# Performance work log

Hardware: AMD Instinct MI355X
Metric: run time of the kernel (lower is better)

## Reference

```python
import jax, jax.numpy as jnp
import numpy as np

N_NODES = 10000
N_EDGES = 640000
IN_CH = 128
HID = 256
OUT_CH = 10
NUM_GRAPHS = 64
EPS = 0.0  # non-trainable buffer, initial_eps=0


def setup_inputs() -> dict:
    key = jax.random.key(0)
    ks = jax.random.split(key, 12)
    x = jax.random.normal(ks[0], (N_NODES, IN_CH), dtype=jnp.float32)
    edge_index = jax.random.randint(ks[1], (2, N_EDGES), 0, N_NODES, dtype=jnp.int64)
    batch = jnp.sort(jax.random.randint(ks[2], (N_NODES,), 0, NUM_GRAPHS, dtype=jnp.int64))
    edge_weights = jax.random.uniform(ks[3], (N_EDGES,), dtype=jnp.float32)
    def lin(k, fan_in, fan_out):
        bound = 1.0 / np.sqrt(fan_in)
        kw, kb = jax.random.split(k)
        W = jax.random.uniform(kw, (fan_out, fan_in), minval=-bound, maxval=bound, dtype=jnp.float32)
        b = jax.random.uniform(kb, (fan_out,), minval=-bound, maxval=bound, dtype=jnp.float32)
        return W, b
    W1, b1 = lin(ks[4], IN_CH, HID)
    W2, b2 = lin(ks[5], HID, HID)
    W3, b3 = lin(ks[6], HID, HID)
    Wl, bl = lin(ks[7], HID, OUT_CH)
    return {"x": x, "edge_index": edge_index, "batch": batch, "edge_weights": edge_weights,
            "W1": W1, "b1": b1, "W2": W2, "b2": b2, "W3": W3, "b3": b3, "Wl": Wl, "bl": bl}


def _ginw_conv(x, edge_index, edge_weights, W, b):
    # message: edge_weight * x_j (source nodes), aggregated by add at target i
    src, dst = edge_index[0], edge_index[1]
    msg = edge_weights[:, None] * x[src]           # [E, F]
    agg = jax.ops.segment_sum(msg, dst, num_segments=N_NODES)  # [N, F]
    out = agg + (1.0 + EPS) * x
    return out @ W.T + b


def reference(x, edge_index, batch, edge_weights, W1, b1, W2, b2, W3, b3, Wl, bl):
    h = jax.nn.relu(_ginw_conv(x, edge_index, edge_weights, W1, b1))
    h = jax.nn.relu(_ginw_conv(h, edge_index, edge_weights, W2, b2))
    h = jax.nn.relu(_ginw_conv(h, edge_index, edge_weights, W3, b3))
    # global mean pool over graphs
    sums = jax.ops.segment_sum(h, batch, num_segments=NUM_GRAPHS)        # [G, HID]
    cnts = jax.ops.segment_sum(jnp.ones((N_NODES,), h.dtype), batch, num_segments=NUM_GRAPHS)
    pooled = sums / jnp.maximum(cnts, 1.0)[:, None]
    return pooled @ Wl.T + bl
```

## Files before the change

### kernel.cpp

```cpp
#include <hip/hip_runtime.h>
#include <hip/hip_fp16.h>

namespace {
constexpr int NN   = 10000;
constexpr int NE   = 640000;
constexpr int INC  = 128;
constexpr int HIDC = 256;
constexpr int OUTC = 10;
constexpr int NG   = 64;
constexpr int DCAP = 128;
}

typedef __attribute__((ext_vector_type(8))) _Float16 half8;
typedef __attribute__((ext_vector_type(4))) float f32x4;
typedef __attribute__((ext_vector_type(4))) ushort u16x4;

__device__ __forceinline__ ushort f2h(float f) { return __half_as_ushort(__float2half(f)); }
__device__ __forceinline__ float h2f(ushort u) { return __half2float(__ushort_as_half(u)); }

__global__ __launch_bounds__(256) void prep_kernel(int* __restrict__ cnt,
                                                   const float* __restrict__ x,
                                                   ushort* __restrict__ xh,
                                                   const float* __restrict__ W1,
                                                   ushort* __restrict__ w1h,
                                                   const float* __restrict__ W2,
                                                   ushort* __restrict__ w2h,
                                                   const float* __restrict__ W3,
                                                   ushort* __restrict__ w3h) {
    const int gt = blockIdx.x * 256 + threadIdx.x;
    const int gs = gridDim.x * 256;
    for (int i = gt; i < NN; i += gs) cnt[i] = 0;
    {
        const int n4 = NN * INC / 4;
        for (int i = gt; i < n4; i += gs) {
            f32x4 v = __builtin_nontemporal_load((const f32x4*)x + i);
            u16x4 o;
#pragma unroll
            for (int j = 0; j < 4; j++) o[j] = f2h(v[j]);
            __builtin_nontemporal_store(o, (u16x4*)xh + i);
        }
    }
    {
        const int n4 = HIDC * INC / 4;
        for (int i = gt; i < n4; i += gs) {
            f32x4 v = __builtin_nontemporal_load((const f32x4*)W1 + i);
            u16x4 o;
#pragma unroll
            for (int j = 0; j < 4; j++) o[j] = f2h(v[j]);
            __builtin_nontemporal_store(o, (u16x4*)w1h + i);
        }
    }
    {
        const int n4 = HIDC * HIDC / 4;
        for (int i = gt; i < n4; i += gs) {
            f32x4 v = __builtin_nontemporal_load((const f32x4*)W2 + i);
            u16x4 o;
#pragma unroll
            for (int j = 0; j < 4; j++) o[j] = f2h(v[j]);
            __builtin_nontemporal_store(o, (u16x4*)w2h + i);
            f32x4 v3 = __builtin_nontemporal_load((const f32x4*)W3 + i);
            u16x4 o3;
#pragma unroll
            for (int j = 0; j < 4; j++) o3[j] = f2h(v3[j]);
            __builtin_nontemporal_store(o3, (u16x4*)w3h + i);
        }
    }
}

__global__ __launch_bounds__(256) void scatter_kernel(const int* __restrict__ ei,
                                                      const float* __restrict__ ew,
                                                      int* __restrict__ cnt,
                                                      uint* __restrict__ erec) {
    const int e = blockIdx.x * 256 + threadIdx.x;
    if (e >= NE) return;
    const int src = __builtin_nontemporal_load(ei + e);
    const int dst = __builtin_nontemporal_load(ei + NE + e);
    const ushort hw = __half_as_ushort(__float2half(__builtin_nontemporal_load(ew + e)));
    const int idx = atomicAdd(&cnt[dst], 1);
    if (idx < DCAP)
        erec[((size_t)dst << 7) + idx] = ((uint)src << 16) | (uint)hw;
}

__global__ __launch_bounds__(256) void gather128_kernel(const int* __restrict__ cnt,
                                                        const uint* __restrict__ erec,
                                                        const ushort* __restrict__ x,
                                                        ushort* __restrict__ out) {
    constexpr int U = 16;
    const int n = blockIdx.x * 4 + (threadIdx.x >> 6);
    const int lane = threadIdx.x & 63;
    if (n >= NN) return;
    const int beg = n << 7;
    const int end = beg + min(cnt[n], DCAP);
    const size_t loff = (size_t)lane * 2;
    const ushort* xr = x + loff;

    float a0, a1, b0 = 0.f, b1 = 0.f;
    {
        ushort2 v = *(const ushort2*)(x + (size_t)n * INC + loff);
        a0 = h2f(v.x);
        a1 = h2f(v.y);
    }

    int e = beg;
    for (; e + U <= end; e += U) {
        uint rec[U];
#pragma unroll
        for (int u = 0; u < U; u++) rec[u] = erec[e + u];
        ushort2 v[U];
#pragma unroll
        for (int u = 0; u < U; u++)
            v[u] = *(const ushort2*)(xr + (size_t)(rec[u] >> 16) * INC);
#pragma unroll
        for (int u = 0; u < U; u++) {
            const float w = h2f((ushort)(rec[u] & 0xFFFFu));
            if (u & 1) { b0 += w * h2f(v[u].x); b1 += w * h2f(v[u].y); }
            else       { a0 += w * h2f(v[u].x); a1 += w * h2f(v[u].y); }
        }
    }
    for (; e < end; e++) {
        const uint rec = erec[e];
        const float w = h2f((ushort)(rec & 0xFFFFu));
        const ushort2 v = *(const ushort2*)(xr + (size_t)(rec >> 16) * INC);
        a0 += w * h2f(v.x);
        a1 += w * h2f(v.y);
    }

    ushort2 o;
    o.x = f2h(a0 + b0);
    o.y = f2h(a1 + b1);
    *(ushort2*)(out + (size_t)n * INC + loff) = o;
}

__global__ __launch_bounds__(256) void gather_half_kernel(const int* __restrict__ cnt,
                                                          const uint* __restrict__ erec,
                                                          const ushort* __restrict__ x,
                                                          ushort* __restrict__ out) {
    constexpr int U = 16;
    const int half = blockIdx.x & 1;
    const int n = (blockIdx.x >> 1) * 4 + (threadIdx.x >> 6);
    const int lane = threadIdx.x & 63;
    if (n >= NN) return;
    const int beg = n << 7;
    const int end = beg + min(cnt[n], DCAP);
    const size_t loff = (size_t)half * 128 + lane * 2;
    const ushort* xr = x + loff;

    float a0, a1, b0 = 0.f, b1 = 0.f;
    {
        ushort2 v = *(const ushort2*)(x + (size_t)n * HIDC + loff);
        a0 = h2f(v.x);
        a1 = h2f(v.y);
    }

    int e = beg;
    for (; e + U <= end; e += U) {
        uint rec[U];
#pragma unroll
        for (int u = 0; u < U; u++) rec[u] = erec[e + u];
        ushort2 v[U];
#pragma unroll
        for (int u = 0; u < U; u++)
            v[u] = *(const ushort2*)(xr + (size_t)(rec[u] >> 16) * HIDC);
#pragma unroll
        for (int u = 0; u < U; u++) {
            const float w = h2f((ushort)(rec[u] & 0xFFFFu));
            if (u & 1) { b0 += w * h2f(v[u].x); b1 += w * h2f(v[u].y); }
            else       { a0 += w * h2f(v[u].x); a1 += w * h2f(v[u].y); }
        }
    }
    for (; e < end; e++) {
        const uint rec = erec[e];
        const float w = h2f((ushort)(rec & 0xFFFFu));
        const ushort2 v = *(const ushort2*)(xr + (size_t)(rec >> 16) * HIDC);
        a0 += w * h2f(v.x);
        a1 += w * h2f(v.y);
    }

    ushort2 o;
    o.x = f2h(a0 + b0);
    o.y = f2h(a1 + b1);
    *(ushort2*)(out + (size_t)n * HIDC + loff) = o;
}

template <int K>
__global__ __launch_bounds__(256) void mfma_gemm_kernel(const ushort* __restrict__ A,
                                                        const ushort* __restrict__ Wb,
                                                        const float* __restrict__ bias,
                                                        ushort* __restrict__ C, int M) {
    constexpr int LDW = K + 8;
    __shared__ ushort Ws[64 * LDW];
    const int tid = threadIdx.x;
    const int bm = blockIdx.x * 128;
    const int bn = blockIdx.y * 64;

    constexpr int CPR = K / 8;
    for (int idx = tid; idx < 64 * CPR; idx += 256) {
        int r = idx / CPR, c = idx % CPR;
        uint4 v = *(const uint4*)(Wb + (size_t)(bn + r) * K + c * 8);
        *(uint4*)(&Ws[r * LDW + c * 8]) = v;
    }
    __syncthreads();

    const int wave = tid >> 6;
    const int lane = tid & 63;
    const int lrow = lane & 15;
    const int lq   = lane >> 4;
    const int m0 = bm + wave * 32;

    f32x4 acc[2][4] = {};
    const int r0 = min(m0 + lrow, M - 1);
    const int r1 = min(m0 + 16 + lrow, M - 1);

    for (int k0 = 0; k0 < K; k0 += 32) {
        const int kk = k0 + lq * 8;
        half8 a0 = __builtin_nontemporal_load((const half8*)(A + (size_t)r0 * K + kk));
        half8 a1 = __builtin_nontemporal_load((const half8*)(A + (size_t)r1 * K + kk));
        half8 b[4];
#pragma unroll
        for (int j = 0; j < 4; j++)
            b[j] = *(const half8*)(&Ws[(j * 16 + lrow) * LDW + kk]);
#pragma unroll
        for (int j = 0; j < 4; j++) {
            acc[0][j] = __builtin_amdgcn_mfma_f32_16x16x32_f16(a0, b[j], acc[0][j], 0, 0, 0);
            acc[1][j] = __builtin_amdgcn_mfma_f32_16x16x32_f16(a1, b[j], acc[1][j], 0, 0, 0);
        }
    }

#pragma unroll
    for (int sub = 0; sub < 2; sub++) {
#pragma unroll
        for (int j = 0; j < 4; j++) {
            const int gn = bn + j * 16 + lrow;
            const float bv = bias[gn];
#pragma unroll
            for (int i = 0; i < 4; i++) {
                const int gm = m0 + sub * 16 + lq * 4 + i;
                if (gm < M) {
                    float v = acc[sub][j][i] + bv;
                    v = fmaxf(v, 0.0f);
                    C[(size_t)gm * HIDC + gn] = f2h(v);
                }
            }
        }
    }
}

__device__ __forceinline__ int lower_bound_batch(const int* __restrict__ batch, int val) {
    int lo = 0, hi = NN;
    while (lo < hi) {
        int mid = (lo + hi) >> 1;
        if (batch[mid] < val) lo = mid + 1;
        else hi = mid;
    }
    return lo;
}

__global__ __launch_bounds__(512) void pool_head_kernel(const ushort* __restrict__ h,
                                                        const int* __restrict__ batch,
                                                        const float* __restrict__ Wl,
                                                        const float* __restrict__ bl,
                                                        float* __restrict__ out) {
    __shared__ float s[8][HIDC];
    __shared__ float s2[OUTC][8];
    const int g = blockIdx.x;
    const int t = threadIdx.x;
    const int p = t >> 6;
    const int c0 = (t & 63) * 4;
    const int lo = lower_bound_batch(batch, g);
    const int hi = lower_bound_batch(batch, g + 1);

    float a0 = 0.f, a1 = 0.f, a2 = 0.f, a3 = 0.f;
    for (int n = lo + p; n < hi; n += 8) {
        u16x4 v = *(const u16x4*)(h + (size_t)n * HIDC + c0);
        a0 += h2f(v[0]); a1 += h2f(v[1]); a2 += h2f(v[2]); a3 += h2f(v[3]);
    }
    s[p][c0 + 0] = a0; s[p][c0 + 1] = a1; s[p][c0 + 2] = a2; s[p][c0 + 3] = a3;
    __syncthreads();

    if (t < HIDC) {
        const float inv = 1.0f / fmaxf((float)(hi - lo), 1.0f);
        float m = 0.f;
#pragma unroll
        for (int q = 0; q < 8; q++) m += s[q][t];
        s[0][t] = m * inv;
    }
    __syncthreads();

    if (t < OUTC * 8) {
        const int oc = t >> 3, q = t & 7;
        float acc = 0.f;
        for (int k = q * 32; k < q * 32 + 32; k++)
            acc += s[0][k] * Wl[(size_t)oc * HIDC + k];
        s2[oc][q] = acc;
    }
    __syncthreads();
    if (t < OUTC) {
        float acc = bl[t];
#pragma unroll
        for (int q = 0; q < 8; q++) acc += s2[t][q];
        out[(size_t)g * OUTC + t] = acc;
    }
}

extern "C" void kernel_launch(void* const* d_in, const int* in_sizes, int n_in,
                              void* d_out, int out_size, void* d_ws, size_t ws_size,
                              hipStream_t stream) {
    const float* x     = (const float*)d_in[0];
    const int*   ei    = (const int*)d_in[1];
    const int*   batch = (const int*)d_in[2];
    const float* ew    = (const float*)d_in[3];
    const float* W1    = (const float*)d_in[4];
    const float* b1    = (const float*)d_in[5];
    const float* W2    = (const float*)d_in[6];
    const float* b2    = (const float*)d_in[7];
    const float* W3    = (const float*)d_in[8];
    const float* b3    = (const float*)d_in[9];
    const float* Wl    = (const float*)d_in[10];
    const float* bl    = (const float*)d_in[11];

    char* p = (char*)d_ws;
    ushort* xh     = (ushort*)p; p += (size_t)NN * INC * 2;
    ushort* agg128 = (ushort*)p; p += (size_t)NN * INC * 2;
    ushort* agg256 = (ushort*)p; p += (size_t)NN * HIDC * 2;
    ushort* h      = (ushort*)p; p += (size_t)NN * HIDC * 2;
    ushort* w1h    = (ushort*)p; p += (size_t)HIDC * INC * 2;
    ushort* w2h    = (ushort*)p; p += (size_t)HIDC * HIDC * 2;
    ushort* w3h    = (ushort*)p; p += (size_t)HIDC * HIDC * 2;
    uint*   erec   = (uint*)p;   p += (size_t)NN * DCAP * 4;
    int*    cnt    = (int*)p;    p += (size_t)NN * 4;

    prep_kernel<<<256, 256, 0, stream>>>(cnt, x, xh, W1, w1h, W2, w2h, W3, w3h);
    scatter_kernel<<<(NE + 255) / 256, 256, 0, stream>>>(ei, ew, cnt, erec);

    const int gather_grid = (NN + 3) / 4;
    dim3 gemm_grid((NN + 127) / 128, HIDC / 64);

    gather128_kernel<<<gather_grid, 256, 0, stream>>>(cnt, erec, xh, agg128);
    mfma_gemm_kernel<INC><<<gemm_grid, 256, 0, stream>>>(agg128, w1h, b1, h, NN);

    gather_half_kernel<<<gather_grid * 2, 256, 0, stream>>>(cnt, erec, h, agg256);
    mfma_gemm_kernel<HIDC><<<gemm_grid, 256, 0, stream>>>(agg256, w2h, b2, h, NN);

    gather_half_kernel<<<gather_grid * 2, 256, 0, stream>>>(cnt, erec, h, agg256);
    mfma_gemm_kernel<HIDC><<<gemm_grid, 256, 0, stream>>>(agg256, w3h, b3, h, NN);

    pool_head_kernel<<<NG, 512, 0, stream>>>(h, batch, Wl, bl, (float*)d_out);
}
```

Before: 261.4 us.

## Restructure CSR build with LDS histograms, widen gathers, fuse pooling into final GEMM

Replaces the global-atomic edge scatter with 16 blocks that each build a shared-memory histogram of destination degrees. Each block then reserves a range per node with one global atomic and fills slots through LDS atomics, while the other blocks run the fp16 conversion of x and the weights in the same launch. The gather kernels now split each wave into two half-waves that handle alternating edges with 4-wide loads and combine them with a cross-lane shuffle. The last GEMM accumulates ReLU outputs straight into per-graph pooled sums through LDS and global float atomics, so the final h is never written back and the head kernel only reads the pooled sums. This adds float-atomic ordering nondeterminism and assumes each 128-row tile covers at most six graphs.

```diff
diff --git a/kernel.cpp b/kernel.cpp
--- a/kernel.cpp
+++ b/kernel.cpp
@@ -9,6 +9,9 @@
 constexpr int OUTC = 10;
 constexpr int NG   = 64;
 constexpr int DCAP = 128;
+constexpr int SB   = 16;
+constexpr int EPB  = NE / SB;
+constexpr int CB   = 240;
 }
 
 typedef __attribute__((ext_vector_type(8))) _Float16 half8;
@@ -18,18 +21,83 @@
 __device__ __forceinline__ ushort f2h(float f) { return __half_as_ushort(__float2half(f)); }
 __device__ __forceinline__ float h2f(ushort u) { return __half2float(__ushort_as_half(u)); }
 
-__global__ __launch_bounds__(256) void prep_kernel(int* __restrict__ cnt,
-                                                   const float* __restrict__ x,
-                                                   ushort* __restrict__ xh,
-                                                   const float* __restrict__ W1,
-                                                   ushort* __restrict__ w1h,
-                                                   const float* __restrict__ W2,
-                                                   ushort* __restrict__ w2h,
-                                                   const float* __restrict__ W3,
-                                                   ushort* __restrict__ w3h) {
+__global__ __launch_bounds__(256) void zero_kernel(int* __restrict__ deg,
+                                                   float* __restrict__ pooled) {
     const int gt = blockIdx.x * 256 + threadIdx.x;
     const int gs = gridDim.x * 256;
-    for (int i = gt; i < NN; i += gs) cnt[i] = 0;
+    for (int i = gt; i < NN; i += gs) deg[i] = 0;
+    for (int i = gt; i < NG * HIDC; i += gs) pooled[i] = 0.0f;
+}
+
+__global__ __launch_bounds__(1024) void build_kernel(const int* __restrict__ ei,
+                                                     const float* __restrict__ ew,
+                                                     int* __restrict__ deg,
+                                                     uint* __restrict__ erec,
+                                                     const float* __restrict__ x,
+                                                     ushort* __restrict__ xh,
+                                                     const float* __restrict__ W1,
+                                                     ushort* __restrict__ w1h,
+                                                     const float* __restrict__ W2,
+                                                     ushort* __restrict__ w2h,
+                                                     const float* __restrict__ W3,
+                                                     ushort* __restrict__ w3h) {
+    __shared__ int hist[NN];
+    const int t = threadIdx.x;
+    const int bid = blockIdx.x;
+
+    if (bid < SB) {
+        const int ebase = bid * EPB;
+        for (int i = t; i < NN; i += 1024) hist[i] = 0;
+        __syncthreads();
+
+        for (int it = 0; it < 10; ++it) {
+            const int vi = it * 4096 + t * 4;
+            if (vi < EPB) {
+                const int4 d4 = *(const int4*)(ei + NE + ebase + vi);
+                atomicAdd(&hist[d4.x], 1);
+                atomicAdd(&hist[d4.y], 1);
+                atomicAdd(&hist[d4.z], 1);
+                atomicAdd(&hist[d4.w], 1);
+            }
+        }
+        __syncthreads();
+
+        for (int b = t; b < NN; b += 1024) {
+            const int c = hist[b];
+            if (c > 0) hist[b] = atomicAdd(&deg[b], c);
+        }
+        __syncthreads();
+
+        for (int it = 0; it < 10; ++it) {
+            const int vi = it * 4096 + t * 4;
+            if (vi < EPB) {
+                const int e = ebase + vi;
+                const int4 s4 = *(const int4*)(ei + e);
+                const int4 d4 = *(const int4*)(ei + NE + e);
+                const float4 w4 = *(const float4*)(ew + e);
+                {
+                    const int idx = atomicAdd(&hist[d4.x], 1);
+                    if (idx < DCAP) erec[((size_t)d4.x << 7) + idx] = ((uint)s4.x << 16) | f2h(w4.x);
+                }
+                {
+                    const int idx = atomicAdd(&hist[d4.y], 1);
+                    if (idx < DCAP) erec[((size_t)d4.y << 7) + idx] = ((uint)s4.y << 16) | f2h(w4.y);
+                }
+                {
+                    const int idx = atomicAdd(&hist[d4.z], 1);
+                    if (idx < DCAP) erec[((size_t)d4.z << 7) + idx] = ((uint)s4.z << 16) | f2h(w4.z);
+                }
+                {
+                    const int idx = atomicAdd(&hist[d4.w], 1);
+                    if (idx < DCAP) erec[((size_t)d4.w << 7) + idx] = ((uint)s4.w << 16) | f2h(w4.w);
+                }
+            }
+        }
+        return;
+    }
+
+    const int gt = (bid - SB) * 1024 + t;
+    const int gs = CB * 1024;
     {
         const int n4 = NN * INC / 4;
         for (int i = gt; i < n4; i += gs) {
@@ -67,119 +135,137 @@
     }
 }
 
-__global__ __launch_bounds__(256) void scatter_kernel(const int* __restrict__ ei,
-                                                      const float* __restrict__ ew,
-                                                      int* __restrict__ cnt,
-                                                      uint* __restrict__ erec) {
-    const int e = blockIdx.x * 256 + threadIdx.x;
-    if (e >= NE) return;
-    const int src = __builtin_nontemporal_load(ei + e);
-    const int dst = __builtin_nontemporal_load(ei + NE + e);
-    const ushort hw = __half_as_ushort(__float2half(__builtin_nontemporal_load(ew + e)));
-    const int idx = atomicAdd(&cnt[dst], 1);
-    if (idx < DCAP)
-        erec[((size_t)dst << 7) + idx] = ((uint)src << 16) | (uint)hw;
-}
-
-__global__ __launch_bounds__(256) void gather128_kernel(const int* __restrict__ cnt,
+__global__ __launch_bounds__(256) void gather128_kernel(const int* __restrict__ deg,
                                                         const uint* __restrict__ erec,
                                                         const ushort* __restrict__ x,
                                                         ushort* __restrict__ out) {
-    constexpr int U = 16;
+    constexpr int U = 8;
     const int n = blockIdx.x * 4 + (threadIdx.x >> 6);
+    if (n >= NN) return;
     const int lane = threadIdx.x & 63;
-    if (n >= NN) return;
+    const int sub = lane >> 5;
+    const int cl  = lane & 31;
+    const int d = min(deg[n], DCAP);
     const int beg = n << 7;
-    const int end = beg + min(cnt[n], DCAP);
-    const size_t loff = (size_t)lane * 2;
+    const size_t loff = (size_t)cl * 4;
     const ushort* xr = x + loff;
 
-    float a0, a1, b0 = 0.f, b1 = 0.f;
+    float a0, a1, a2, a3;
     {
-        ushort2 v = *(const ushort2*)(x + (size_t)n * INC + loff);
-        a0 = h2f(v.x);
-        a1 = h2f(v.y);
-    }
-
-    int e = beg;
-    for (; e + U <= end; e += U) {
+        u16x4 v = *(const u16x4*)(x + (size_t)n * INC + loff);
+        a0 = sub ? 0.f : h2f(v[0]);
+        a1 = sub ? 0.f : h2f(v[1]);
+        a2 = sub ? 0.f : h2f(v[2]);
+        a3 = sub ? 0.f : h2f(v[3]);
+    }
+
+    int e = 0;
+    for (; e + 2 * U <= d; e += 2 * U) {
         uint rec[U];
 #pragma unroll
-        for (int u = 0; u < U; u++) rec[u] = erec[e + u];
-        ushort2 v[U];
+        for (int u = 0; u < U; u++) rec[u] = erec[beg + e + 2 * u + sub];
+        u16x4 v[U];
 #pragma unroll
         for (int u = 0; u < U; u++)
-            v[u] = *(const ushort2*)(xr + (size_t)(rec[u] >> 16) * INC);
+            v[u] = *(const u16x4*)(xr + (size_t)(rec[u] >> 16) * INC);
 #pragma unroll
         for (int u = 0; u < U; u++) {
             const float w = h2f((ushort)(rec[u] & 0xFFFFu));
-            if (u & 1) { b0 += w * h2f(v[u].x); b1 += w * h2f(v[u].y); }
-            else       { a0 += w * h2f(v[u].x); a1 += w * h2f(v[u].y); }
-        }
-    }
-    for (; e < end; e++) {
-        const uint rec = erec[e];
+            a0 += w * h2f(v[u][0]);
+            a1 += w * h2f(v[u][1]);
+            a2 += w * h2f(v[u][2]);
+            a3 += w * h2f(v[u][3]);
+        }
+    }
+    for (; e + 2 <= d; e += 2) {
+        const uint rec = erec[beg + e + sub];
         const float w = h2f((ushort)(rec & 0xFFFFu));
-        const ushort2 v = *(const ushort2*)(xr + (size_t)(rec >> 16) * INC);
-        a0 += w * h2f(v.x);
-        a1 += w * h2f(v.y);
-    }
-
-    ushort2 o;
-    o.x = f2h(a0 + b0);
-    o.y = f2h(a1 + b1);
-    *(ushort2*)(out + (size_t)n * INC + loff) = o;
-}
-
-__global__ __launch_bounds__(256) void gather_half_kernel(const int* __restrict__ cnt,
+        const u16x4 v = *(const u16x4*)(xr + (size_t)(rec >> 16) * INC);
+        a0 += w * h2f(v[0]); a1 += w * h2f(v[1]); a2 += w * h2f(v[2]); a3 += w * h2f(v[3]);
+    }
+    if (e < d && sub == 0) {
+        const uint rec = erec[beg + e];
+        const float w = h2f((ushort)(rec & 0xFFFFu));
+        const u16x4 v = *(const u16x4*)(xr + (size_t)(rec >> 16) * INC);
+        a0 += w * h2f(v[0]); a1 += w * h2f(v[1]); a2 += w * h2f(v[2]); a3 += w * h2f(v[3]);
+    }
+
+    a0 += __shfl_xor(a0, 32, 64);
+    a1 += __shfl_xor(a1, 32, 64);
+    a2 += __shfl_xor(a2, 32, 64);
+    a3 += __shfl_xor(a3, 32, 64);
+    if (sub == 0) {
+        u16x4 o;
+        o[0] = f2h(a0); o[1] = f2h(a1); o[2] = f2h(a2); o[3] = f2h(a3);
+        __builtin_nontemporal_store(o, (u16x4*)(out + (size_t)n * INC + loff));
+    }
+}
+
+__global__ __launch_bounds__(256) void gather_half_kernel(const int* __restrict__ deg,
                                                           const uint* __restrict__ erec,
                                                           const ushort* __restrict__ x,
                                                           ushort* __restrict__ out) {
-    constexpr int U = 16;
+    constexpr int U = 8;
     const int half = blockIdx.x & 1;
     const int n = (blockIdx.x >> 1) * 4 + (threadIdx.x >> 6);
+    if (n >= NN) return;
     const int lane = threadIdx.x & 63;
-    if (n >= NN) return;
+    const int sub = lane >> 5;
+    const int cl  = lane & 31;
+    const int d = min(deg[n], DCAP);
     const int beg = n << 7;
-    const int end = beg + min(cnt[n], DCAP);
-    const size_t loff = (size_t)half * 128 + lane * 2;
+    const size_t loff = (size_t)half * 128 + cl * 4;
     const ushort* xr = x + loff;
 
-    float a0, a1, b0 = 0.f, b1 = 0.f;
+    float a0, a1, a2, a3;
     {
-        ushort2 v = *(const ushort2*)(x + (size_t)n * HIDC + loff);
-        a0 = h2f(v.x);
-        a1 = h2f(v.y);
-    }
-
-    int e = beg;
-    for (; e + U <= end; e += U) {
+        u16x4 v = *(const u16x4*)(x + (size_t)n * HIDC + loff);
+        a0 = sub ? 0.f : h2f(v[0]);
+        a1 = sub ? 0.f : h2f(v[1]);
+        a2 = sub ? 0.f : h2f(v[2]);
+        a3 = sub ? 0.f : h2f(v[3]);
+    }
+
+    int e = 0;
+    for (; e + 2 * U <= d; e += 2 * U) {
         uint rec[U];
 #pragma unroll
-        for (int u = 0; u < U; u++) rec[u] = erec[e + u];
-        ushort2 v[U];
+        for (int u = 0; u < U; u++) rec[u] = erec[beg + e + 2 * u + sub];
+        u16x4 v[U];
 #pragma unroll
         for (int u = 0; u < U; u++)
-            v[u] = *(const ushort2*)(xr + (size_t)(rec[u] >> 16) * HIDC);
+            v[u] = *(const u16x4*)(xr + (size_t)(rec[u] >> 16) * HIDC);
 #pragma unroll
         for (int u = 0; u < U; u++) {
             const float w = h2f((ushort)(rec[u] & 0xFFFFu));
-            if (u & 1) { b0 += w * h2f(v[u].x); b1 += w * h2f(v[u].y); }
-            else       { a0 += w * h2f(v[u].x); a1 += w * h2f(v[u].y); }
-        }
-    }
-    for (; e < end; e++) {
-        const uint rec = erec[e];
+            a0 += w * h2f(v[u][0]);
+            a1 += w * h2f(v[u][1]);
+            a2 += w * h2f(v[u][2]);
+            a3 += w * h2f(v[u][3]);
+        }
+    }
+    for (; e + 2 <= d; e += 2) {
+        const uint rec = erec[beg + e + sub];
         const float w = h2f((ushort)(rec & 0xFFFFu));
-        const ushort2 v = *(const ushort2*)(xr + (size_t)(rec >> 16) * HIDC);
-        a0 += w * h2f(v.x);
-        a1 += w * h2f(v.y);
-    }
-
-    ushort2 o;
-    o.x = f2h(a0 + b0);
-    o.y = f2h(a1 + b1);
-    *(ushort2*)(out + (size_t)n * HIDC + loff) = o;
+        const u16x4 v = *(const u16x4*)(xr + (size_t)(rec >> 16) * HIDC);
+        a0 += w * h2f(v[0]); a1 += w * h2f(v[1]); a2 += w * h2f(v[2]); a3 += w * h2f(v[3]);
+    }
+    if (e < d && sub == 0) {
+        const uint rec = erec[beg + e];
+        const float w = h2f((ushort)(rec & 0xFFFFu));
+        const u16x4 v = *(const u16x4*)(xr + (size_t)(rec >> 16) * HIDC);
+        a0 += w * h2f(v[0]); a1 += w * h2f(v[1]); a2 += w * h2f(v[2]); a3 += w * h2f(v[3]);
+    }
+
+    a0 += __shfl_xor(a0, 32, 64);
+    a1 += __shfl_xor(a1, 32, 64);
+    a2 += __shfl_xor(a2, 32, 64);
+    a3 += __shfl_xor(a3, 32, 64);
+    if (sub == 0) {
+        u16x4 o;
+        o[0] = f2h(a0); o[1] = f2h(a1); o[2] = f2h(a2); o[3] = f2h(a3);
+        __builtin_nontemporal_store(o, (u16x4*)(out + (size_t)n * HIDC + loff));
+    }
 }
 
 template <int K>
@@ -245,6 +331,82 @@
     }
 }
 
+__global__ __launch_bounds__(256) void mfma_gemm_pool_kernel(const ushort* __restrict__ A,
+                                                             const ushort* __restrict__ Wb,
+                                                             const float* __restrict__ bias,
+                                                             const int* __restrict__ batch,
+                                                             float* __restrict__ pooled, int M) {
+    constexpr int K = HIDC;
+    constexpr int LDW = K + 8;
+    __shared__ ushort Ws[64 * LDW];
+    __shared__ float pl[6][64];
+    const int tid = threadIdx.x;
+    const int bm = blockIdx.x * 128;
+    const int bn = blockIdx.y * 64;
+
+    constexpr int CPR = K / 8;
+    for (int idx = tid; idx < 64 * CPR; idx += 256) {
+        int r = idx / CPR, c = idx % CPR;
+        uint4 v = *(const uint4*)(Wb + (size_t)(bn + r) * K + c * 8);
+        *(uint4*)(&Ws[r * LDW + c * 8]) = v;
+    }
+    for (int i = tid; i < 6 * 64; i += 256) pl[i >> 6][i & 63] = 0.0f;
+    __syncthreads();
+
+    const int wave = tid >> 6;
+    const int lane = tid & 63;
+    const int lrow = lane & 15;
+    const int lq   = lane >> 4;
+    const int m0 = bm + wave * 32;
+    const int g0 = batch[bm];
+
+    f32x4 acc[2][4] = {};
+    const int r0 = min(m0 + lrow, M - 1);
+    const int r1 = min(m0 + 16 + lrow, M - 1);
+
+    for (int k0 = 0; k0 < K; k0 += 32) {
+        const int kk = k0 + lq * 8;
+        half8 a0 = __builtin_nontemporal_load((const half8*)(A + (size_t)r0 * K + kk));
+        half8 a1 = __builtin_nontemporal_load((const half8*)(A + (size_t)r1 * K + kk));
+        half8 b[4];
+#pragma unroll
+        for (int j = 0; j < 4; j++)
+            b[j] = *(const half8*)(&Ws[(j * 16 + lrow) * LDW + kk]);
+#pragma unroll
+        for (int j = 0; j < 4; j++) {
+            acc[0][j] = __builtin_amdgcn_mfma_f32_16x16x32_f16(a0, b[j], acc[0][j], 0, 0, 0);
+            acc[1][j] = __builtin_amdgcn_mfma_f32_16x16x32_f16(a1, b[j], acc[1][j], 0, 0, 0);
+        }
+    }
+
+#pragma unroll
+    for (int sub = 0; sub < 2; sub++) {
+#pragma unroll
+        for (int i = 0; i < 4; i++) {
+            const int gm = m0 + sub * 16 + lq * 4 + i;
+            if (gm < M) {
+                const int gi = min(batch[gm] - g0, 5);
+#pragma unroll
+                for (int j = 0; j < 4; j++) {
+                    const int gn = bn + j * 16 + lrow;
+                    float v = acc[sub][j][i] + bias[gn];
+                    v = fmaxf(v, 0.0f);
+                    atomicAdd(&pl[gi][j * 16 + lrow], v);
+                }
+            }
+        }
+    }
+    __syncthreads();
+
+    for (int i = tid; i < 6 * 64; i += 256) {
+        const int s = i >> 6, col = i & 63;
+        const float v = pl[s][col];
+        const int gg = g0 + s;
+        if (v != 0.0f && gg < NG)
+            atomicAdd(&pooled[(size_t)gg * HIDC + bn + col], v);
+    }
+}
+
 __device__ __forceinline__ int lower_bound_batch(const int* __restrict__ batch, int val) {
     int lo = 0, hi = NN;
     while (lo < hi) {
@@ -255,42 +417,26 @@
     return lo;
 }
 
-__global__ __launch_bounds__(512) void pool_head_kernel(const ushort* __restrict__ h,
-                                                        const int* __restrict__ batch,
-                                                        const float* __restrict__ Wl,
-                                                        const float* __restrict__ bl,
-                                                        float* __restrict__ out) {
-    __shared__ float s[8][HIDC];
+__global__ __launch_bounds__(256) void head_kernel(const float* __restrict__ pooled,
+                                                   const int* __restrict__ batch,
+                                                   const float* __restrict__ Wl,
+                                                   const float* __restrict__ bl,
+                                                   float* __restrict__ out) {
+    __shared__ float s[HIDC];
     __shared__ float s2[OUTC][8];
     const int g = blockIdx.x;
     const int t = threadIdx.x;
-    const int p = t >> 6;
-    const int c0 = (t & 63) * 4;
     const int lo = lower_bound_batch(batch, g);
     const int hi = lower_bound_batch(batch, g + 1);
-
-    float a0 = 0.f, a1 = 0.f, a2 = 0.f, a3 = 0.f;
-    for (int n = lo + p; n < hi; n += 8) {
-        u16x4 v = *(const u16x4*)(h + (size_t)n * HIDC + c0);
-        a0 += h2f(v[0]); a1 += h2f(v[1]); a2 += h2f(v[2]); a3 += h2f(v[3]);
-    }
-    s[p][c0 + 0] = a0; s[p][c0 + 1] = a1; s[p][c0 + 2] = a2; s[p][c0 + 3] = a3;
-    __syncthreads();
-
-    if (t < HIDC) {
-        const float inv = 1.0f / fmaxf((float)(hi - lo), 1.0f);
-        float m = 0.f;
-#pragma unroll
-        for (int q = 0; q < 8; q++) m += s[q][t];
-        s[0][t] = m * inv;
-    }
+    const float inv = 1.0f / fmaxf((float)(hi - lo), 1.0f);
+    if (t < HIDC) s[t] = pooled[(size_t)g * HIDC + t] * inv;
     __syncthreads();
 
     if (t < OUTC * 8) {
         const int oc = t >> 3, q = t & 7;
         float acc = 0.f;
         for (int k = q * 32; k < q * 32 + 32; k++)
-            acc += s[0][k] * Wl[(size_t)oc * HIDC + k];
+            acc += s[k] * Wl[(size_t)oc * HIDC + k];
         s2[oc][q] = acc;
     }
     __syncthreads();
@@ -327,22 +473,24 @@
     ushort* w2h    = (ushort*)p; p += (size_t)HIDC * HIDC * 2;
     ushort* w3h    = (ushort*)p; p += (size_t)HIDC * HIDC * 2;
     uint*   erec   = (uint*)p;   p += (size_t)NN * DCAP * 4;
-    int*    cnt    = (int*)p;    p += (size_t)NN * 4;
-
-    prep_kernel<<<256, 256, 0, stream>>>(cnt, x, xh, W1, w1h, W2, w2h, W3, w3h);
-    scatter_kernel<<<(NE + 255) / 256, 256, 0, stream>>>(ei, ew, cnt, erec);
+    int*    deg    = (int*)p;    p += (size_t)NN * 4;
+    float*  pooled = (float*)p;  p += (size_t)NG * HIDC * 4;
+
+    zero_kernel<<<32, 256, 0, stream>>>(deg, pooled);
+    build_kernel<<<SB + CB, 1024, 0, stream>>>(ei, ew, deg, erec, x, xh,
+                                               W1, w1h, W2, w2h, W3, w3h);
 
     const int gather_grid = (NN + 3) / 4;
     dim3 gemm_grid((NN + 127) / 128, HIDC / 64);
 
-    gather128_kernel<<<gather_grid, 256, 0, stream>>>(cnt, erec, xh, agg128);
+    gather128_kernel<<<gather_grid, 256, 0, stream>>>(deg, erec, xh, agg128);
     mfma_gemm_kernel<INC><<<gemm_grid, 256, 0, stream>>>(agg128, w1h, b1, h, NN);
 
-    gather_half_kernel<<<gather_grid * 2, 256, 0, stream>>>(cnt, erec, h, agg256);
+    gather_half_kernel<<<gather_grid * 2, 256, 0, stream>>>(deg, erec, h, agg256);
     mfma_gemm_kernel<HIDC><<<gemm_grid, 256, 0, stream>>>(agg256, w2h, b2, h, NN);
 
-    gather_half_kernel<<<gather_grid * 2, 256, 0, stream>>>(cnt, erec, h, agg256);
-    mfma_gemm_kernel<HIDC><<<gemm_grid, 256, 0, stream>>>(agg256, w3h, b3, h, NN);
-
-    pool_head_kernel<<<NG, 512, 0, stream>>>(h, batch, Wl, bl, (float*)d_out);
-}
+    gather_half_kernel<<<gather_grid * 2, 256, 0, stream>>>(deg, erec, h, agg256);
+    mfma_gemm_pool_kernel<<<gemm_grid, 256, 0, stream>>>(agg256, w3h, b3, batch, pooled, NN);
+
+    head_kernel<<<NG, 256, 0, stream>>>(pooled, batch, Wl, bl, (float*)d_out);
+}
```

Result: no change. 265.4 us (+1.5%).
